# Kernel optimization log

Hardware: AMD Instinct MI355X
Metric: run time of the kernel (lower is better)

Reference implementation:

```python
import jax, jax.numpy as jnp
import numpy as np

B, N, C = 8, 512, 256
HID_E = 32          # edge_pred hidden width
FILTERS = (64, 64, 64)
OUT = 2


def setup_inputs() -> dict:
    key = jax.random.key(0)
    ks = jax.random.split(key, 12)
    s = 0.05
    inp = {
        "x": jax.random.normal(ks[0], (B, N, C), jnp.float32),
        "A": jax.random.uniform(ks[1], (B, N, N), jnp.float32),
        "mask": jnp.ones((B, N), jnp.float32),
        # edge predictor: Linear(2C,32) -> ReLU -> Linear(32,1)
        "ew1": jax.random.normal(ks[2], (2 * C, HID_E), jnp.float32) * s,
        "eb1": jnp.zeros((HID_E,), jnp.float32),
        "ew2": jax.random.normal(ks[3], (HID_E, 1), jnp.float32) * s,
        "eb2": jnp.zeros((1,), jnp.float32),
        # GraphConv stack: Linear(in*n_relations, f) per layer (n_relations=2)
        "gw0": jax.random.normal(ks[4], (2 * C, FILTERS[0]), jnp.float32) * s,
        "gb0": jnp.zeros((FILTERS[0],), jnp.float32),
        "gw1": jax.random.normal(ks[5], (2 * FILTERS[0], FILTERS[1]), jnp.float32) * s,
        "gb1": jnp.zeros((FILTERS[1],), jnp.float32),
        "gw2": jax.random.normal(ks[6], (2 * FILTERS[1], FILTERS[2]), jnp.float32) * s,
        "gb2": jnp.zeros((FILTERS[2],), jnp.float32),
        # final classifier (dropout is identity in eval)
        "fcw": jax.random.normal(ks[7], (FILTERS[2], OUT), jnp.float32) * s,
        "fcb": jnp.zeros((OUT,), jnp.float32),
    }
    return inp


def _laplacian(A):
    # A_hat = A + I ; L = D^-1/2 A_hat D^-1/2 with D from row-sums (dim 1)
    n = A.shape[-1]
    A_hat = A + jnp.eye(n, dtype=A.dtype)
    D = (A_hat.sum(axis=1) + 1e-5) ** -0.5  # [B,N]
    return D[:, :, None] * A_hat * D[:, None, :]


def reference(x, A, mask, ew1, eb1, ew2, eb2, gw0, gb0, gw1, gb1, gw2, gb2, fcw, fcb):
    b, n, c = x.shape
    # edge MLP over all node pairs; first layer split so we never build [B,N,N,2C]
    wa, wb = ew1[:c], ew1[c:]
    xa = x @ wa  # [B,N,32] contribution of node i
    xb = x @ wb  # [B,N,32] contribution of node j
    h = jax.nn.relu(xa[:, :, None, :] + xb[:, None, :, :] + eb1)  # [B,N,N,32]
    e = (h @ ew2)[..., 0] + eb2[0]  # e[b,i,j] = edge_pred([x_i, x_j])
    # symmetrized score: exp(0.5 * (f(i,j) + f(j,i)))
    y = jnp.exp(0.5 * (e + jnp.swapaxes(e, 1, 2)))
    triu = jnp.triu(jnp.ones((n, n), bool), 1)
    valid = (mask[:, :, None] > 0) & (mask[:, None, :] > 0)
    A_pred = jnp.where(triu[None] & valid, y, 0.0)
    A_pred = A_pred + jnp.swapaxes(A_pred, 1, 2)

    # multi-relation GCN stack (relations: input A, predicted A_pred)
    L0 = _laplacian(A)
    L1 = _laplacian(A_pred)
    m = mask[:, :, None]
    h0 = x
    for W, bias in ((gw0, gb0), (gw1, gb1), (gw2, gb2)):
        xh = jnp.concatenate([L0 @ h0, L1 @ h0], axis=-1)  # [B,N,2*f_in]
        h0 = jax.nn.relu((xh @ W + bias) * m)
    g = h0.max(axis=1)  # [B, filters[-1]] global max pool over nodes
    return g @ fcw + fcb  # [B, OUT]
```

## Files before the change

kernel.cpp:

```cpp
#include <hip/hip_runtime.h>
#include <hip/hip_bf16.h>
#include <math.h>

#define NB 8
#define NN 512
#define NC 256
#define HID 32

typedef __attribute__((ext_vector_type(8))) short short8;
typedef __attribute__((ext_vector_type(4))) float float4v;
typedef unsigned short ushort_t;

__device__ __forceinline__ ushort_t f2bf(float x) {
    unsigned u = __float_as_uint(x);
    return (ushort_t)((u + 0x7fffu + ((u >> 16) & 1u)) >> 16);
}
__device__ __forceinline__ float bf2f(ushort_t h) {
    return __uint_as_float(((unsigned)h) << 16);
}

__global__ __launch_bounds__(256) void xaxb_gemm(
    const float* __restrict__ x, const float* __restrict__ ew1,
    const float* __restrict__ eb1, float* __restrict__ xab,
    float* __restrict__ dsum, unsigned* __restrict__ gmax, int* __restrict__ done)
{
    __shared__ float sX[32][17];
    __shared__ float sW[32][68];
    int t = threadIdx.x;
    if (blockIdx.x < 32) dsum[blockIdx.x * 256 + t] = 0.f;
    if (blockIdx.x == 32) {
        gmax[t] = 0u; gmax[t + 256] = 0u;
        if (t < NB) done[t] = 0;
    }
    int r0 = blockIdx.x * 16;
    int tx = t & 15, ty = t >> 4;
    float acc[4] = {0.f, 0.f, 0.f, 0.f};
    for (int k0 = 0; k0 < NC; k0 += 32) {
        {
            int kk = (t & 15) * 2, r = t >> 4;
            float2 v = *(const float2*)(x + (size_t)(r0 + r) * NC + k0 + kk);
            sX[kk][r] = v.x; sX[kk + 1][r] = v.y;
        }
        {
            int c4 = (t & 15) * 4;
            int half = c4 >> 5, cc = c4 & 31;
#pragma unroll
            for (int rr = 0; rr < 2; ++rr) {
                int kk = (t >> 4) + rr * 16;
                *(float4*)&sW[kk][c4] =
                    *(const float4*)(ew1 + (size_t)(half * NC + k0 + kk) * HID + cc);
            }
        }
        __syncthreads();
#pragma unroll
        for (int k = 0; k < 32; ++k) {
            float a = sX[k][ty];
            float4 w = *(const float4*)&sW[k][tx * 4];
            acc[0] = fmaf(a, w.x, acc[0]); acc[1] = fmaf(a, w.y, acc[1]);
            acc[2] = fmaf(a, w.z, acc[2]); acc[3] = fmaf(a, w.w, acc[3]);
        }
        __syncthreads();
    }
    int c4 = tx * 4;
    float4 o; o.x = acc[0]; o.y = acc[1]; o.z = acc[2]; o.w = acc[3];
    if (c4 >= 32) {
        o.x += eb1[c4 - 32]; o.y += eb1[c4 - 31];
        o.z += eb1[c4 - 30]; o.w += eb1[c4 - 29];
    }
    *(float4*)&xab[(size_t)(r0 + ty) * 64 + c4] = o;
}

__global__ __launch_bounds__(256) void edge_scores(
    const float* __restrict__ xab, const float* __restrict__ ew2,
    const float* __restrict__ eb2, const float* __restrict__ mask,
    const float* __restrict__ A, ushort_t* __restrict__ Ah,
    ushort_t* __restrict__ APh, float* __restrict__ dsum)
{
    __shared__ float sI[32][65], sJ[32][65];
    __shared__ float sV[32][33];
    __shared__ float w2[32];
    int b = blockIdx.z;
    int p = blockIdx.x;
    int X = 0;
    while ((X + 1) * 16 - ((X + 1) * X) / 2 <= p) ++X;
    int Y = X + (p - (X * 16 - (X * (X - 1)) / 2));
    int i0 = X * 32, j0 = Y * 32;
    int t = threadIdx.x;
    if (t < 32) w2[t] = ew2[t];
    {
        int c4 = (t & 15) * 4;
#pragma unroll
        for (int rr = 0; rr < 2; ++rr) {
            int r = (t >> 4) + rr * 16;
            float4 vi = *(const float4*)(xab + ((size_t)(b * NN + i0 + r)) * 64 + c4);
            float4 vj = *(const float4*)(xab + ((size_t)(b * NN + j0 + r)) * 64 + c4);
            sI[r][c4] = vi.x; sI[r][c4 + 1] = vi.y; sI[r][c4 + 2] = vi.z; sI[r][c4 + 3] = vi.w;
            sJ[r][c4] = vj.x; sJ[r][c4 + 1] = vj.y; sJ[r][c4 + 2] = vj.z; sJ[r][c4 + 3] = vj.w;
        }
    }
    __syncthreads();
    float eb2v = eb2[0];
#pragma unroll
    for (int pz = 0; pz < 4; ++pz) {
        int e = t + pz * 256;
        int ti = e >> 5, tj = e & 31;
        int i = i0 + ti, j = j0 + tj;
        float sij = 0.f, sji = 0.f;
#pragma unroll
        for (int k = 0; k < 32; ++k) {
            sij = fmaf(fmaxf(sI[ti][k] + sJ[tj][32 + k], 0.f), w2[k], sij);
            sji = fmaf(fmaxf(sJ[tj][k] + sI[ti][32 + k], 0.f), w2[k], sji);
        }
        bool ok = (i != j) && (mask[b * NN + i] > 0.f) && (mask[b * NN + j] > 0.f);
        sV[ti][tj] = ok ? expf(0.5f * (sij + sji) + eb2v) : 0.f;
    }
    __syncthreads();
#pragma unroll
    for (int pz = 0; pz < 4; ++pz) {
        int r = (t >> 5) + pz * 8, c = t & 31;
        size_t o1 = ((size_t)(b * NN + i0 + r)) * NN + j0 + c;
        size_t o2 = ((size_t)(b * NN + j0 + r)) * NN + i0 + c;
        APh[o1] = f2bf(sV[r][c]);
        APh[o2] = f2bf(sV[c][r]);
    }
    if (t < 32) {
        float s = 0.f;
#pragma unroll
        for (int r = 0; r < 32; ++r) s += sV[r][t];
        atomicAdd(&dsum[(NB * NN) + b * NN + j0 + t], s);
    } else if (t < 64 && X != Y) {
        int c = t - 32;
        float s = 0.f;
#pragma unroll
        for (int j = 0; j < 32; ++j) s += sV[c][j];
        atomicAdd(&dsum[(NB * NN) + b * NN + i0 + c], s);
    }
    if (p < 128) {
        const float* Ar = A + ((size_t)b * NN + 4 * p) * NN;
        ushort_t* Hr = Ah + ((size_t)b * NN + 4 * p) * NN;
        float s0 = 0.f, s1 = 0.f;
#pragma unroll
        for (int rr = 0; rr < 4; ++rr) {
            float a0 = Ar[(size_t)rr * NN + t];
            float a1 = Ar[(size_t)rr * NN + t + 256];
            Hr[(size_t)rr * NN + t] = f2bf(a0);
            Hr[(size_t)rr * NN + t + 256] = f2bf(a1);
            s0 += a0; s1 += a1;
        }
        atomicAdd(&dsum[b * NN + t], s0);
        atomicAdd(&dsum[b * NN + t + 256], s1);
    }
}

__global__ __launch_bounds__(256) void pre_gemmT(
    const float* __restrict__ h, const float* __restrict__ gw,
    const float* __restrict__ dsum, ushort_t* __restrict__ PTh, int Cin)
{
    __shared__ float sH[32][17];
    __shared__ float sW[32][132];
    __shared__ __align__(16) ushort_t sTh[128][24];
    int r0 = blockIdx.x * 16;
    int t = threadIdx.x;
    int tx = t & 31, ty = t >> 5;
    float acc0[4] = {0.f, 0.f, 0.f, 0.f};
    float acc1[4] = {0.f, 0.f, 0.f, 0.f};
    for (int k0 = 0; k0 < Cin; k0 += 32) {
        {
            int kk = (t & 15) * 2, r = t >> 4;
            float2 v = *(const float2*)(h + (size_t)(r0 + r) * Cin + k0 + kk);
            sH[kk][r] = v.x; sH[kk + 1][r] = v.y;
        }
        {
            int c4 = (t & 31) * 4;
            int half = c4 >> 6, cc = c4 & 63;
#pragma unroll
            for (int rr = 0; rr < 4; ++rr) {
                int kk = (t >> 5) + rr * 8;
                *(float4*)&sW[kk][c4] =
                    *(const float4*)(gw + (size_t)(half * Cin + k0 + kk) * 64 + cc);
            }
        }
        __syncthreads();
#pragma unroll
        for (int k = 0; k < 32; ++k) {
            float a0 = sH[k][ty * 2];
            float a1 = sH[k][ty * 2 + 1];
            float4 w = *(const float4*)&sW[k][tx * 4];
            acc0[0] = fmaf(a0, w.x, acc0[0]); acc0[1] = fmaf(a0, w.y, acc0[1]);
            acc0[2] = fmaf(a0, w.z, acc0[2]); acc0[3] = fmaf(a0, w.w, acc0[3]);
            acc1[0] = fmaf(a1, w.x, acc1[0]); acc1[1] = fmaf(a1, w.y, acc1[1]);
            acc1[2] = fmaf(a1, w.z, acc1[2]); acc1[3] = fmaf(a1, w.w, acc1[3]);
        }
        __syncthreads();
    }
    int c4 = tx * 4;
    const float* draw = dsum + ((c4 >= 64) ? (NB * NN) : 0);
#pragma unroll
    for (int r = 0; r < 2; ++r) {
        int rl = ty * 2 + r;
        int row = r0 + rl;
        float d = rsqrtf(draw[row] + 1.0f + 1e-5f);
        float* ap = (r == 0) ? acc0 : acc1;
#pragma unroll
        for (int n = 0; n < 4; ++n)
            sTh[c4 + n][rl] = f2bf(d * ap[n]);
    }
    __syncthreads();
    {
        int c = t & 127, half = t >> 7;
        int bb = r0 >> 9, ibase = r0 & (NN - 1);
        ushort_t* dst = PTh + ((size_t)(bb * 128 + c)) * NN + ibase + half * 8;
        *(short8*)dst = *(const short8*)&sTh[c][half * 8];
    }
}

__global__ __launch_bounds__(256) void fused_layer(
    const ushort_t* __restrict__ Ah, const ushort_t* __restrict__ APh,
    const ushort_t* __restrict__ Pa, const ushort_t* __restrict__ Pb,
    ushort_t* __restrict__ Qa, ushort_t* __restrict__ Qb,
    const float* __restrict__ dsum, const float* __restrict__ gb,
    const float* __restrict__ mask, const float* __restrict__ gwN,
    unsigned* __restrict__ gmax, int* __restrict__ done,
    const float* __restrict__ fcw, const float* __restrict__ fcb,
    float* __restrict__ out, int dualP, int mode)
{
    __shared__ union {
        struct { ushort_t sA[2][16][72]; ushort_t sP1[64][72]; ushort_t sP2[64][72]; } a;
        struct { ushort_t sWT[128][40]; } b;
    } u;
    __shared__ float sRed[2][32][17];
    __shared__ float sH16[16][36];
    __shared__ float sD[2][16];
    __shared__ int lastFlag;

    int t = threadIdx.x;
    int b = blockIdx.z, ch = blockIdx.y, i0 = blockIdx.x * 16;
    int lane = t & 63, w = t >> 6;
    int quad = lane >> 4, m16 = lane & 15;
    int lap = w >> 1, cg = w & 1;

    int sa_arr = t >> 7, sa_id = t & 127;
    int sa_r = sa_id >> 3, sa_q = sa_id & 7;
    const ushort_t* sa_src = (sa_arr ? APh : Ah)
        + ((size_t)(b * NN + i0 + sa_r)) * NN + sa_q * 8;
    float4v acc = {0.f, 0.f, 0.f, 0.f};

    for (int k0 = 0; k0 < NN; k0 += 64) {
        __syncthreads();
        *(short8*)&u.a.sA[sa_arr][sa_r][sa_q * 8] = *(const short8*)(sa_src + k0);
#pragma unroll
        for (int cc2 = 0; cc2 < 2; ++cc2) {
            int chunk = t + cc2 * 256;
            int l = chunk >> 3, q = chunk & 7;
            int colg = (l >> 5) * 64 + ch * 32 + (l & 31);
            size_t off = ((size_t)(b * 128 + colg)) * NN + k0 + q * 8;
            *(short8*)&u.a.sP1[l][q * 8] = *(const short8*)(Pa + off);
            if (dualP)
                *(short8*)&u.a.sP2[l][q * 8] = *(const short8*)(Pb + off);
        }
        __syncthreads();
#pragma unroll
        for (int kh = 0; kh < 2; ++kh) {
            int ko = kh * 32 + quad * 8;
            short8 av = *(const short8*)&u.a.sA[lap][m16][ko];
            short8 p1 = *(const short8*)&u.a.sP1[w * 16 + m16][ko];
            acc = __builtin_amdgcn_mfma_f32_16x16x32_bf16(p1, av, acc, 0, 0, 0);
            if (dualP) {
                short8 p2 = *(const short8*)&u.a.sP2[w * 16 + m16][ko];
                acc = __builtin_amdgcn_mfma_f32_16x16x32_bf16(p2, av, acc, 0, 0, 0);
            }
        }
    }
    int gi = b * NN + i0 + m16;
    float d = rsqrtf(dsum[lap * (NB * NN) + gi] + 1.0f + 1e-5f);
    if (cg == 0 && quad == 0) sD[lap][m16] = d;
    int cbase = cg * 16 + quad * 4;
#pragma unroll
    for (int r = 0; r < 4; ++r) {
        int c32 = cbase + r;
        int pcol = lap * 64 + ch * 32 + c32;
        size_t pidx = ((size_t)(b * 128 + pcol)) * NN + i0 + m16;
        float pv = bf2f(Pa[pidx]);
        if (dualP) pv += bf2f(Pb[pidx]);
        sRed[lap][c32][m16] = d * (acc[r] + pv);
    }
    __syncthreads();
#pragma unroll
    for (int s = 0; s < 2; ++s) {
        int idx = t + s * 256;
        int c32 = idx & 31, i = idx >> 5;
        float mv = mask[b * NN + i0 + i];
        float v = (sRed[0][c32][i] + sRed[1][c32][i] + gb[ch * 32 + c32]) * mv;
        sH16[i][c32] = fmaxf(v, 0.f);
    }
    __syncthreads();

    if (mode == 0) {
#pragma unroll
        for (int kk = 0; kk < 8; ++kk) {
            int chunk = t + kk * 256;
            int c = chunk & 127;
            int k = (chunk >> 7) * 2;
            int base = (c < 64) ? (ch * 32) : (64 + ch * 32);
            int gc = c & 63;
            float f0 = gwN[(size_t)(base + k) * 64 + gc];
            float f1 = gwN[(size_t)(base + k + 1) * 64 + gc];
            unsigned pk = (unsigned)f2bf(f0) | ((unsigned)f2bf(f1) << 16);
            *(unsigned*)&u.b.sWT[c][k] = pk;
        }
        __syncthreads();
        float4 h0 = *(const float4*)&sH16[m16][quad * 8];
        float4 h1 = *(const float4*)&sH16[m16][quad * 8 + 4];
        short8 bf;
        bf[0] = f2bf(h0.x); bf[1] = f2bf(h0.y); bf[2] = f2bf(h0.z); bf[3] = f2bf(h0.w);
        bf[4] = f2bf(h1.x); bf[5] = f2bf(h1.y); bf[6] = f2bf(h1.z); bf[7] = f2bf(h1.w);
        ushort_t* Q = ch ? Qb : Qa;
#pragma unroll
        for (int s2 = 0; s2 < 2; ++s2) {
            int ctile = w * 2 + s2;
            short8 af = *(const short8*)&u.b.sWT[ctile * 16 + m16][quad * 8];
            float4v dacc = {0.f, 0.f, 0.f, 0.f};
            dacc = __builtin_amdgcn_mfma_f32_16x16x32_bf16(af, bf, dacc, 0, 0, 0);
            float dsc = sD[(ctile >= 4) ? 1 : 0][m16];
#pragma unroll
            for (int r = 0; r < 4; ++r) {
                int c = ctile * 16 + quad * 4 + r;
                Q[((size_t)(b * 128 + c)) * NN + i0 + m16] = f2bf(dsc * dacc[r]);
            }
        }
    } else {
        if (t < 32) {
            float mx = 0.f;
#pragma unroll
            for (int r = 0; r < 16; ++r) mx = fmaxf(mx, sH16[r][t]);
            atomicMax(&gmax[b * 64 + ch * 32 + t], __float_as_uint(mx));
        }
        __syncthreads();
        if (t == 0) {
            __threadfence();
            int old = atomicAdd(&done[b], 1);
            lastFlag = (old == 63);
        }
        __syncthreads();
        if (lastFlag) {
            if (t < 64) {
                unsigned ub = __hip_atomic_load(&gmax[b * 64 + t],
                                                __ATOMIC_RELAXED,
                                                __HIP_MEMORY_SCOPE_AGENT);
                ((float*)sRed)[t] = __uint_as_float(ub);
            }
            __syncthreads();
            if (t < 2) {
                float a2 = fcb[t];
#pragma unroll
                for (int k = 0; k < 64; ++k)
                    a2 = fmaf(((float*)sRed)[k], fcw[k * 2 + t], a2);
                out[b * 2 + t] = a2;
            }
        }
    }
}

extern "C" void kernel_launch(void* const* d_in, const int* in_sizes, int n_in,
                              void* d_out, int out_size, void* d_ws, size_t ws_size,
                              hipStream_t stream)
{
    const float* x    = (const float*)d_in[0];
    const float* A    = (const float*)d_in[1];
    const float* mask = (const float*)d_in[2];
    const float* ew1  = (const float*)d_in[3];
    const float* eb1  = (const float*)d_in[4];
    const float* ew2  = (const float*)d_in[5];
    const float* eb2  = (const float*)d_in[6];
    const float* gw0  = (const float*)d_in[7];
    const float* gb0  = (const float*)d_in[8];
    const float* gw1  = (const float*)d_in[9];
    const float* gb1  = (const float*)d_in[10];
    const float* gw2  = (const float*)d_in[11];
    const float* gb2  = (const float*)d_in[12];
    const float* fcw  = (const float*)d_in[13];
    const float* fcb  = (const float*)d_in[14];
    float* out = (float*)d_out;
    char* ws = (char*)d_ws;

    const size_t NEL = (size_t)NB * NN * NN;
    const size_t PSL = (size_t)NB * 128 * NN;
    float*    xab  = (float*)ws;                   ws += 262144 * 4;
    ushort_t* APh  = (ushort_t*)ws;                ws += NEL * 2;
    ushort_t* Ahs  = (ushort_t*)ws;                ws += NEL * 2;
    float*    dsum = (float*)ws;                   ws += 8192 * 4;
    ushort_t* PT_A = (ushort_t*)ws;                ws += PSL * 2;
    ushort_t* PB1a = (ushort_t*)ws;                ws += PSL * 2;
    ushort_t* PB1b = (ushort_t*)ws;                ws += PSL * 2;
    ushort_t* PB2a = (ushort_t*)ws;                ws += PSL * 2;
    ushort_t* PB2b = (ushort_t*)ws;                ws += PSL * 2;
    unsigned* gmax = (unsigned*)ws;                ws += 512 * 4;
    int*      done = (int*)ws;                     ws += 64 * 4;

    xaxb_gemm  <<<256, 256, 0, stream>>>(x, ew1, eb1, xab, dsum, gmax, done);
    edge_scores<<<dim3(136, 1, NB), 256, 0, stream>>>(xab, ew2, eb2, mask,
                                                      A, Ahs, APh, dsum);
    pre_gemmT  <<<256, 256, 0, stream>>>(x, gw0, dsum, PT_A, 256);

    fused_layer<<<dim3(32, 2, NB), 256, 0, stream>>>(
        Ahs, APh, PT_A, PT_A, PB1a, PB1b, dsum, gb0, mask, gw1,
        gmax, done, fcw, fcb, out, 0, 0);
    fused_layer<<<dim3(32, 2, NB), 256, 0, stream>>>(
        Ahs, APh, PB1a, PB1b, PB2a, PB2b, dsum, gb1, mask, gw2,
        gmax, done, fcw, fcb, out, 1, 0);
    fused_layer<<<dim3(32, 2, NB), 256, 0, stream>>>(
        Ahs, APh, PB2a, PB2b, PB2a, PB2b, dsum, gb2, mask, gw2,
        gmax, done, fcw, fcb, out, 1, 1);
}
```

Measured before the change: 171.8 us.

## Merge first-layer projection into front GEMM kernel and prefetch tiles in fused layer

The separate pre_gemmT launch is folded into the front GEMM kernel, which now runs 512 blocks: the first 256 compute the edge-MLP projections and the rest compute the unscaled x@gw0 projection. Because that projection no longer waits for dsum from edge_scores, the degree scaling is applied inside the first fused_layer when tiles are staged into shared memory (scaleP flag). The fused_layer K loop and the front GEMMs now use register prefetch of the next tile to overlap global loads with MFMA/FMA work. The cost is an extra bf16 round-trip during scaling, more registers, and a 4 KB shared-memory degree table.

```diff
diff --git a/kernel.cpp b/kernel.cpp
--- a/kernel.cpp
+++ b/kernel.cpp
@@ -19,55 +19,118 @@
     return __uint_as_float(((unsigned)h) << 16);
 }
 
-__global__ __launch_bounds__(256) void xaxb_gemm(
+__global__ __launch_bounds__(256) void front_gemms(
     const float* __restrict__ x, const float* __restrict__ ew1,
-    const float* __restrict__ eb1, float* __restrict__ xab,
+    const float* __restrict__ eb1, const float* __restrict__ gw0,
+    float* __restrict__ xab, ushort_t* __restrict__ T0,
     float* __restrict__ dsum, unsigned* __restrict__ gmax, int* __restrict__ done)
 {
-    __shared__ float sX[32][17];
-    __shared__ float sW[32][68];
+    __shared__ __align__(16) union {
+        struct { float sX[32][17]; float sW[32][68]; } a;
+        struct { float sH[32][17]; float sW[32][132]; ushort_t sTh[128][24]; } b;
+    } u;
     int t = threadIdx.x;
-    if (blockIdx.x < 32) dsum[blockIdx.x * 256 + t] = 0.f;
-    if (blockIdx.x == 32) {
-        gmax[t] = 0u; gmax[t + 256] = 0u;
-        if (t < NB) done[t] = 0;
-    }
-    int r0 = blockIdx.x * 16;
-    int tx = t & 15, ty = t >> 4;
-    float acc[4] = {0.f, 0.f, 0.f, 0.f};
-    for (int k0 = 0; k0 < NC; k0 += 32) {
+
+    if (blockIdx.x < 256) {
+        if (blockIdx.x < 32) dsum[blockIdx.x * 256 + t] = 0.f;
+        if (blockIdx.x == 32) {
+            gmax[t] = 0u; gmax[t + 256] = 0u;
+            if (t < NB) done[t] = 0;
+        }
+        int r0 = blockIdx.x * 16;
+        int tx = t & 15, ty = t >> 4;
+        int xk = (t & 15) * 2, xr = t >> 4;
+        int c4 = (t & 15) * 4;
+        int whalf = c4 >> 5, wcc = c4 & 31;
+        float acc[4] = {0.f, 0.f, 0.f, 0.f};
+
+        float2 rx = *(const float2*)(x + (size_t)(r0 + xr) * NC + xk);
+        float4 rw0 = *(const float4*)(ew1 + (size_t)(whalf * NC + xr) * HID + wcc);
+        float4 rw1 = *(const float4*)(ew1 + (size_t)(whalf * NC + xr + 16) * HID + wcc);
+
+        for (int k0 = 0; k0 < NC; k0 += 32) {
+            u.a.sX[xk][xr] = rx.x; u.a.sX[xk + 1][xr] = rx.y;
+            *(float4*)&u.a.sW[xr][c4] = rw0;
+            *(float4*)&u.a.sW[xr + 16][c4] = rw1;
+            if (k0 + 32 < NC) {
+                rx  = *(const float2*)(x + (size_t)(r0 + xr) * NC + k0 + 32 + xk);
+                rw0 = *(const float4*)(ew1 + (size_t)(whalf * NC + k0 + 32 + xr) * HID + wcc);
+                rw1 = *(const float4*)(ew1 + (size_t)(whalf * NC + k0 + 32 + xr + 16) * HID + wcc);
+            }
+            __syncthreads();
+#pragma unroll
+            for (int k = 0; k < 32; ++k) {
+                float a = u.a.sX[k][ty];
+                float4 w = *(const float4*)&u.a.sW[k][tx * 4];
+                acc[0] = fmaf(a, w.x, acc[0]); acc[1] = fmaf(a, w.y, acc[1]);
+                acc[2] = fmaf(a, w.z, acc[2]); acc[3] = fmaf(a, w.w, acc[3]);
+            }
+            __syncthreads();
+        }
+        int oc4 = tx * 4;
+        float4 o; o.x = acc[0]; o.y = acc[1]; o.z = acc[2]; o.w = acc[3];
+        if (oc4 >= 32) {
+            o.x += eb1[oc4 - 32]; o.y += eb1[oc4 - 31];
+            o.z += eb1[oc4 - 30]; o.w += eb1[oc4 - 29];
+        }
+        *(float4*)&xab[(size_t)(r0 + ty) * 64 + oc4] = o;
+    } else {
+        int r0 = (blockIdx.x - 256) * 16;
+        int tx = t & 31, ty = t >> 5;
+        int xk = (t & 15) * 2, xr = t >> 4;
+        int c4w = (t & 31) * 4;
+        int whalf = c4w >> 6, wcc = c4w & 63;
+        int wk = t >> 5;
+        float acc0[4] = {0.f, 0.f, 0.f, 0.f};
+        float acc1[4] = {0.f, 0.f, 0.f, 0.f};
+
+        float2 rx = *(const float2*)(x + (size_t)(r0 + xr) * NC + xk);
+        float4 rw[4];
+#pragma unroll
+        for (int rr = 0; rr < 4; ++rr)
+            rw[rr] = *(const float4*)(gw0 + (size_t)(whalf * NC + wk + rr * 8) * 64 + wcc);
+
+        for (int k0 = 0; k0 < NC; k0 += 32) {
+            u.b.sH[xk][xr] = rx.x; u.b.sH[xk + 1][xr] = rx.y;
+#pragma unroll
+            for (int rr = 0; rr < 4; ++rr)
+                *(float4*)&u.b.sW[wk + rr * 8][c4w] = rw[rr];
+            if (k0 + 32 < NC) {
+                rx = *(const float2*)(x + (size_t)(r0 + xr) * NC + k0 + 32 + xk);
+#pragma unroll
+                for (int rr = 0; rr < 4; ++rr)
+                    rw[rr] = *(const float4*)(gw0 + (size_t)(whalf * NC + k0 + 32 + wk + rr * 8) * 64 + wcc);
+            }
+            __syncthreads();
+#pragma unroll
+            for (int k = 0; k < 32; ++k) {
+                float a0 = u.b.sH[k][ty * 2];
+                float a1 = u.b.sH[k][ty * 2 + 1];
+                float4 w = *(const float4*)&u.b.sW[k][tx * 4];
+                acc0[0] = fmaf(a0, w.x, acc0[0]); acc0[1] = fmaf(a0, w.y, acc0[1]);
+                acc0[2] = fmaf(a0, w.z, acc0[2]); acc0[3] = fmaf(a0, w.w, acc0[3]);
+                acc1[0] = fmaf(a1, w.x, acc1[0]); acc1[1] = fmaf(a1, w.y, acc1[1]);
+                acc1[2] = fmaf(a1, w.z, acc1[2]); acc1[3] = fmaf(a1, w.w, acc1[3]);
+            }
+            __syncthreads();
+        }
+        int c4 = tx * 4;
+#pragma unroll
+        for (int r = 0; r < 2; ++r) {
+            int rl = ty * 2 + r;
+            float* ap = (r == 0) ? acc0 : acc1;
+#pragma unroll
+            for (int n = 0; n < 4; ++n)
+                u.b.sTh[c4 + n][rl] = f2bf(ap[n]);
+        }
+        __syncthreads();
         {
-            int kk = (t & 15) * 2, r = t >> 4;
-            float2 v = *(const float2*)(x + (size_t)(r0 + r) * NC + k0 + kk);
-            sX[kk][r] = v.x; sX[kk + 1][r] = v.y;
-        }
-        {
-            int c4 = (t & 15) * 4;
-            int half = c4 >> 5, cc = c4 & 31;
-#pragma unroll
-            for (int rr = 0; rr < 2; ++rr) {
-                int kk = (t >> 4) + rr * 16;
-                *(float4*)&sW[kk][c4] =
-                    *(const float4*)(ew1 + (size_t)(half * NC + k0 + kk) * HID + cc);
-            }
-        }
-        __syncthreads();
-#pragma unroll
-        for (int k = 0; k < 32; ++k) {
-            float a = sX[k][ty];
-            float4 w = *(const float4*)&sW[k][tx * 4];
-            acc[0] = fmaf(a, w.x, acc[0]); acc[1] = fmaf(a, w.y, acc[1]);
-            acc[2] = fmaf(a, w.z, acc[2]); acc[3] = fmaf(a, w.w, acc[3]);
-        }
-        __syncthreads();
-    }
-    int c4 = tx * 4;
-    float4 o; o.x = acc[0]; o.y = acc[1]; o.z = acc[2]; o.w = acc[3];
-    if (c4 >= 32) {
-        o.x += eb1[c4 - 32]; o.y += eb1[c4 - 31];
-        o.z += eb1[c4 - 30]; o.w += eb1[c4 - 29];
-    }
-    *(float4*)&xab[(size_t)(r0 + ty) * 64 + c4] = o;
+            int c = t & 127, half = t >> 7;
+            int bb = r0 >> 9, ibase = r0 & (NN - 1);
+            ushort_t* dst = T0 + ((size_t)(bb * 128 + c)) * NN + ibase + half * 8;
+            *(short8*)dst = *(const short8*)&u.b.sTh[c][half * 8];
+        }
+    }
 }
 
 __global__ __launch_bounds__(256) void edge_scores(
@@ -152,68 +215,6 @@
     }
 }
 
-__global__ __launch_bounds__(256) void pre_gemmT(
-    const float* __restrict__ h, const float* __restrict__ gw,
-    const float* __restrict__ dsum, ushort_t* __restrict__ PTh, int Cin)
-{
-    __shared__ float sH[32][17];
-    __shared__ float sW[32][132];
-    __shared__ __align__(16) ushort_t sTh[128][24];
-    int r0 = blockIdx.x * 16;
-    int t = threadIdx.x;
-    int tx = t & 31, ty = t >> 5;
-    float acc0[4] = {0.f, 0.f, 0.f, 0.f};
-    float acc1[4] = {0.f, 0.f, 0.f, 0.f};
-    for (int k0 = 0; k0 < Cin; k0 += 32) {
-        {
-            int kk = (t & 15) * 2, r = t >> 4;
-            float2 v = *(const float2*)(h + (size_t)(r0 + r) * Cin + k0 + kk);
-            sH[kk][r] = v.x; sH[kk + 1][r] = v.y;
-        }
-        {
-            int c4 = (t & 31) * 4;
-            int half = c4 >> 6, cc = c4 & 63;
-#pragma unroll
-            for (int rr = 0; rr < 4; ++rr) {
-                int kk = (t >> 5) + rr * 8;
-                *(float4*)&sW[kk][c4] =
-                    *(const float4*)(gw + (size_t)(half * Cin + k0 + kk) * 64 + cc);
-            }
-        }
-        __syncthreads();
-#pragma unroll
-        for (int k = 0; k < 32; ++k) {
-            float a0 = sH[k][ty * 2];
-            float a1 = sH[k][ty * 2 + 1];
-            float4 w = *(const float4*)&sW[k][tx * 4];
-            acc0[0] = fmaf(a0, w.x, acc0[0]); acc0[1] = fmaf(a0, w.y, acc0[1]);
-            acc0[2] = fmaf(a0, w.z, acc0[2]); acc0[3] = fmaf(a0, w.w, acc0[3]);
-            acc1[0] = fmaf(a1, w.x, acc1[0]); acc1[1] = fmaf(a1, w.y, acc1[1]);
-            acc1[2] = fmaf(a1, w.z, acc1[2]); acc1[3] = fmaf(a1, w.w, acc1[3]);
-        }
-        __syncthreads();
-    }
-    int c4 = tx * 4;
-    const float* draw = dsum + ((c4 >= 64) ? (NB * NN) : 0);
-#pragma unroll
-    for (int r = 0; r < 2; ++r) {
-        int rl = ty * 2 + r;
-        int row = r0 + rl;
-        float d = rsqrtf(draw[row] + 1.0f + 1e-5f);
-        float* ap = (r == 0) ? acc0 : acc1;
-#pragma unroll
-        for (int n = 0; n < 4; ++n)
-            sTh[c4 + n][rl] = f2bf(d * ap[n]);
-    }
-    __syncthreads();
-    {
-        int c = t & 127, half = t >> 7;
-        int bb = r0 >> 9, ibase = r0 & (NN - 1);
-        ushort_t* dst = PTh + ((size_t)(bb * 128 + c)) * NN + ibase + half * 8;
-        *(short8*)dst = *(const short8*)&sTh[c][half * 8];
-    }
-}
-
 __global__ __launch_bounds__(256) void fused_layer(
     const ushort_t* __restrict__ Ah, const ushort_t* __restrict__ APh,
     const ushort_t* __restrict__ Pa, const ushort_t* __restrict__ Pb,
@@ -222,7 +223,7 @@
     const float* __restrict__ mask, const float* __restrict__ gwN,
     unsigned* __restrict__ gmax, int* __restrict__ done,
     const float* __restrict__ fcw, const float* __restrict__ fcb,
-    float* __restrict__ out, int dualP, int mode)
+    float* __restrict__ out, int dualP, int mode, int scaleP)
 {
     __shared__ union {
         struct { ushort_t sA[2][16][72]; ushort_t sP1[64][72]; ushort_t sP2[64][72]; } a;
@@ -231,6 +232,7 @@
     __shared__ float sRed[2][32][17];
     __shared__ float sH16[16][36];
     __shared__ float sD[2][16];
+    __shared__ __align__(16) float sDj[2][NN];
     __shared__ int lastFlag;
 
     int t = threadIdx.x;
@@ -239,24 +241,68 @@
     int quad = lane >> 4, m16 = lane & 15;
     int lap = w >> 1, cg = w & 1;
 
+    if (scaleP) {
+#pragma unroll
+        for (int s = 0; s < 4; ++s) {
+            int idx = t + s * 256;
+            int lp = idx >> 9, j = idx & (NN - 1);
+            sDj[lp][j] = rsqrtf(dsum[lp * (NB * NN) + b * NN + j] + 1.0f + 1e-5f);
+        }
+    }
+
     int sa_arr = t >> 7, sa_id = t & 127;
     int sa_r = sa_id >> 3, sa_q = sa_id & 7;
     const ushort_t* sa_src = (sa_arr ? APh : Ah)
         + ((size_t)(b * NN + i0 + sa_r)) * NN + sa_q * 8;
+    int pl0 = t >> 3, pq = t & 7;
+    size_t poff0 = ((size_t)(b * 128 + ch * 32 + pl0)) * NN + pq * 8;
+    size_t poff1 = ((size_t)(b * 128 + 64 + ch * 32 + pl0)) * NN + pq * 8;
+
     float4v acc = {0.f, 0.f, 0.f, 0.f};
 
+    short8 rA   = *(const short8*)(sa_src);
+    short8 rP1a = *(const short8*)(Pa + poff0);
+    short8 rP1b = *(const short8*)(Pa + poff1);
+    short8 rP2a = rP1a, rP2b = rP1b;
+    if (dualP) {
+        rP2a = *(const short8*)(Pb + poff0);
+        rP2b = *(const short8*)(Pb + poff1);
+    }
+
     for (int k0 = 0; k0 < NN; k0 += 64) {
         __syncthreads();
-        *(short8*)&u.a.sA[sa_arr][sa_r][sa_q * 8] = *(const short8*)(sa_src + k0);
-#pragma unroll
-        for (int cc2 = 0; cc2 < 2; ++cc2) {
-            int chunk = t + cc2 * 256;
-            int l = chunk >> 3, q = chunk & 7;
-            int colg = (l >> 5) * 64 + ch * 32 + (l & 31);
-            size_t off = ((size_t)(b * 128 + colg)) * NN + k0 + q * 8;
-            *(short8*)&u.a.sP1[l][q * 8] = *(const short8*)(Pa + off);
-            if (dualP)
-                *(short8*)&u.a.sP2[l][q * 8] = *(const short8*)(Pb + off);
+        *(short8*)&u.a.sA[sa_arr][sa_r][sa_q * 8] = rA;
+        if (scaleP) {
+            float4v d0a = *(const float4v*)&sDj[0][k0 + pq * 8];
+            float4v d0b = *(const float4v*)&sDj[0][k0 + pq * 8 + 4];
+            float4v d1a = *(const float4v*)&sDj[1][k0 + pq * 8];
+            float4v d1b = *(const float4v*)&sDj[1][k0 + pq * 8 + 4];
+            short8 w0, w1;
+#pragma unroll
+            for (int e = 0; e < 4; ++e) {
+                w0[e]     = (short)f2bf(bf2f((ushort_t)rP1a[e])     * d0a[e]);
+                w0[e + 4] = (short)f2bf(bf2f((ushort_t)rP1a[e + 4]) * d0b[e]);
+                w1[e]     = (short)f2bf(bf2f((ushort_t)rP1b[e])     * d1a[e]);
+                w1[e + 4] = (short)f2bf(bf2f((ushort_t)rP1b[e + 4]) * d1b[e]);
+            }
+            *(short8*)&u.a.sP1[pl0][pq * 8] = w0;
+            *(short8*)&u.a.sP1[32 + pl0][pq * 8] = w1;
+        } else {
+            *(short8*)&u.a.sP1[pl0][pq * 8] = rP1a;
+            *(short8*)&u.a.sP1[32 + pl0][pq * 8] = rP1b;
+            if (dualP) {
+                *(short8*)&u.a.sP2[pl0][pq * 8] = rP2a;
+                *(short8*)&u.a.sP2[32 + pl0][pq * 8] = rP2b;
+            }
+        }
+        if (k0 + 64 < NN) {
+            rA   = *(const short8*)(sa_src + k0 + 64);
+            rP1a = *(const short8*)(Pa + poff0 + k0 + 64);
+            rP1b = *(const short8*)(Pa + poff1 + k0 + 64);
+            if (dualP) {
+                rP2a = *(const short8*)(Pb + poff0 + k0 + 64);
+                rP2b = *(const short8*)(Pb + poff1 + k0 + 64);
+            }
         }
         __syncthreads();
 #pragma unroll
@@ -282,6 +328,7 @@
         size_t pidx = ((size_t)(b * 128 + pcol)) * NN + i0 + m16;
         float pv = bf2f(Pa[pidx]);
         if (dualP) pv += bf2f(Pb[pidx]);
+        if (scaleP) pv *= d;
         sRed[lap][c32][m16] = d * (acc[r] + pv);
     }
     __syncthreads();
@@ -397,18 +444,18 @@
     unsigned* gmax = (unsigned*)ws;                ws += 512 * 4;
     int*      done = (int*)ws;                     ws += 64 * 4;
 
-    xaxb_gemm  <<<256, 256, 0, stream>>>(x, ew1, eb1, xab, dsum, gmax, done);
+    front_gemms<<<512, 256, 0, stream>>>(x, ew1, eb1, gw0, xab, PT_A,
+                                         dsum, gmax, done);
     edge_scores<<<dim3(136, 1, NB), 256, 0, stream>>>(xab, ew2, eb2, mask,
                                                       A, Ahs, APh, dsum);
-    pre_gemmT  <<<256, 256, 0, stream>>>(x, gw0, dsum, PT_A, 256);
 
     fused_layer<<<dim3(32, 2, NB), 256, 0, stream>>>(
         Ahs, APh, PT_A, PT_A, PB1a, PB1b, dsum, gb0, mask, gw1,
-        gmax, done, fcw, fcb, out, 0, 0);
+        gmax, done, fcw, fcb, out, 0, 0, 1);
     fused_layer<<<dim3(32, 2, NB), 256, 0, stream>>>(
         Ahs, APh, PB1a, PB1b, PB2a, PB2b, dsum, gb1, mask, gw2,
-        gmax, done, fcw, fcb, out, 1, 0);
+        gmax, done, fcw, fcb, out, 1, 0, 0);
     fused_layer<<<dim3(32, 2, NB), 256, 0, stream>>>(
         Ahs, APh, PB2a, PB2b, PB2a, PB2b, dsum, gb2, mask, gw2,
-        gmax, done, fcw, fcb, out, 1, 1);
-}
+        gmax, done, fcw, fcb, out, 1, 1, 0);
+}
```

Result: faster. 161.2 us (-6.2%).
